# Kernel tuning notes

Hardware: AMD Instinct MI355X
Metric: run time of the kernel (lower is better)

Reference implementation:

```python
import jax, jax.numpy as jnp
import numpy as np

N_USERS = 200000
N_SPOTS = 50000
N_EDGES = 3200000
D = 64


def setup_inputs() -> dict:
    key = jax.random.key(0)
    k1, k2, k3, k4 = jax.random.split(key, 4)
    return {
        "user_x": jax.random.normal(k1, (N_USERS, D), dtype=jnp.float32),
        "spot_x": jax.random.normal(k2, (N_SPOTS, D), dtype=jnp.float32),
        "user_idx": jax.random.randint(k3, (N_EDGES,), 0, N_USERS, dtype=jnp.int32),
        "spot_idx": jax.random.randint(k4, (N_EDGES,), 0, N_SPOTS, dtype=jnp.int32),
    }


def reference(user_x, spot_x, user_idx, spot_idx):
    n_users, n_spots = user_x.shape[0], spot_x.shape[0]
    dtype = user_x.dtype
    ones = jnp.ones(user_idx.shape[0], dtype=dtype)
    # per-node degrees (counts of edge endpoints); isolated nodes get 1e-6
    user_div = jax.ops.segment_sum(ones, user_idx, num_segments=n_users)
    spot_div = jax.ops.segment_sum(ones, spot_idx, num_segments=n_spots)
    user_div = jnp.where(user_div == 0, jnp.asarray(1e-6, dtype), user_div)
    spot_div = jnp.where(spot_div == 0, jnp.asarray(1e-6, dtype), spot_div)
    inv_sqrt_user = jax.lax.rsqrt(user_div)  # [n_users]
    inv_sqrt_spot = jax.lax.rsqrt(spot_div)  # [n_spots]
    # gather + pre-normalize per-edge messages
    spot_msg = spot_x[spot_idx] * inv_sqrt_spot[spot_idx][:, None]  # [E, D]
    user_msg = user_x[user_idx] * inv_sqrt_user[user_idx][:, None]  # [E, D]
    # scatter-add into destination nodes, then post-normalize by dest degree
    spot_out = jax.ops.segment_sum(user_msg, spot_idx, num_segments=n_spots)
    user_out = jax.ops.segment_sum(spot_msg, user_idx, num_segments=n_users)
    spot_out = spot_out * inv_sqrt_spot[:, None]
    user_out = user_out * inv_sqrt_user[:, None]
    return (user_out, spot_out)
```

## Files before the change

### kernel.cpp

```cpp
#include <hip/hip_runtime.h>

#define DFEAT  64
#define BSH    7
#define BN     128
#define PBITS  18
#define PMASK  ((1u << PBITS) - 1)
#define NSPLIT 384
#define STR_U  2560
#define STR_S  9216


__device__ __forceinline__ long long bucket_base(int b, int NB_U) {
    return (b < NB_U) ? (long long)b * STR_U
                      : (long long)NB_U * STR_U + (long long)(b - NB_U) * STR_S;
}

__global__ __launch_bounds__(256) void split_kernel(const int* __restrict__ uidx,
                                                    const int* __restrict__ sidx,
                                                    int* __restrict__ cursor,
                                                    unsigned int* __restrict__ staging,
                                                    int n_edges, int NB_U, int NB) {
    __shared__ int h[2048];
    __shared__ int rc[2048];
    for (int i = threadIdx.x; i < NB; i += 256) h[i] = 0;
    __syncthreads();
    int epb = (((n_edges + gridDim.x - 1) / gridDim.x) + 3) & ~3;
    int e0 = blockIdx.x * epb;
    int e1 = min(e0 + epb, n_edges);
    int len = e1 - e0; if (len < 0) len = 0;
    int nv = e0 + (len & ~3);
    for (int v = e0 + 4 * (int)threadIdx.x; v < nv; v += 1024) {
        int4 u = *(const int4*)(uidx + v);
        int4 s = *(const int4*)(sidx + v);
        atomicAdd(&h[u.x >> BSH], 1); atomicAdd(&h[u.y >> BSH], 1);
        atomicAdd(&h[u.z >> BSH], 1); atomicAdd(&h[u.w >> BSH], 1);
        atomicAdd(&h[NB_U + (s.x >> BSH)], 1); atomicAdd(&h[NB_U + (s.y >> BSH)], 1);
        atomicAdd(&h[NB_U + (s.z >> BSH)], 1); atomicAdd(&h[NB_U + (s.w >> BSH)], 1);
    }
    for (int e = nv + (int)threadIdx.x; e < e1; e += 256) {
        atomicAdd(&h[uidx[e] >> BSH], 1);
        atomicAdd(&h[NB_U + (sidx[e] >> BSH)], 1);
    }
    __syncthreads();
    for (int i = threadIdx.x; i < NB; i += 256) {
        int c = h[i];
        rc[i] = c ? (int)(bucket_base(i, NB_U) + atomicAdd(&cursor[i], c)) : 0;
    }
    __syncthreads();
    for (int v = e0 + 4 * (int)threadIdx.x; v < nv; v += 1024) {
        int4 u4 = *(const int4*)(uidx + v);
        int4 s4 = *(const int4*)(sidx + v);
#pragma unroll
        for (int k = 0; k < 4; ++k) {
            int u = ((const int*)&u4)[k];
            int s = ((const int*)&s4)[k];
            int pu = atomicAdd(&rc[u >> BSH], 1);
            staging[pu] = ((unsigned int)(u & (BN - 1)) << PBITS) | (unsigned int)s;
            int ps = atomicAdd(&rc[NB_U + (s >> BSH)], 1);
            staging[ps] = ((unsigned int)(s & (BN - 1)) << PBITS) | (unsigned int)u;
        }
    }
    for (int e = nv + (int)threadIdx.x; e < e1; e += 256) {
        int u = uidx[e], s = sidx[e];
        int pu = atomicAdd(&rc[u >> BSH], 1);
        staging[pu] = ((unsigned int)(u & (BN - 1)) << PBITS) | (unsigned int)s;
        int ps = atomicAdd(&rc[NB_U + (s >> BSH)], 1);
        staging[ps] = ((unsigned int)(s & (BN - 1)) << PBITS) | (unsigned int)u;
    }
}

template <int CAPN>
__global__ __launch_bounds__(256) void csr_build_inplace_t(
        unsigned int* __restrict__ staging,
        const int* __restrict__ cursor,
        int* __restrict__ start,
        int* __restrict__ cnt,
        float* __restrict__ isq,
        int n_users, int n_spots,
        int NB_U, int b0) {
    __shared__ unsigned int buf[CAPN];
    __shared__ int hist[BN];
    __shared__ int scanbuf[BN];
    __shared__ int cur[BN];
    int b = b0 + blockIdx.x, t = threadIdx.x;
    long long beg = bucket_base(b, NB_U);
    int len = cursor[b];
    if (len > CAPN) len = CAPN;
    if (t < BN) hist[t] = 0;
    __syncthreads();
    for (int i = t; i < len; i += 256) {
        unsigned int e = __builtin_nontemporal_load(&staging[beg + i]);
        buf[i] = e;
        atomicAdd(&hist[e >> PBITS], 1);
    }
    __syncthreads();
    if (t < BN) scanbuf[t] = hist[t];
    __syncthreads();
    for (int off = 1; off < BN; off <<= 1) {
        int v = (t >= off && t < BN) ? scanbuf[t - off] : 0;
        __syncthreads();
        if (t < BN) scanbuf[t] += v;
        __syncthreads();
    }
    if (t < BN) {
        int excl = scanbuf[t] - hist[t];
        cur[t] = (int)beg + excl;
        bool ub = (b < NB_U);
        int node = (ub ? (b << BSH) : ((b - NB_U) << BSH)) + t;
        int lim  = ub ? n_users : n_spots;
        if (node < lim) {
            int gi = ub ? node : (n_users + node);
            start[gi] = (int)beg + excl;
            cnt[gi]   = hist[t];
            float d = hist[t] ? (float)hist[t] : 1e-6f;
            isq[gi] = rsqrtf(d);
        }
    }
    __syncthreads();
    for (int i = t; i < len; i += 256) {
        unsigned int e = buf[i];
        int pos = atomicAdd(&cur[e >> PBITS], 1);
        staging[pos] = e & PMASK;
    }
}

__global__ __launch_bounds__(256) void scale_feat(const float* __restrict__ ux,
                                                  const float* __restrict__ sx,
                                                  const float* __restrict__ isq,
                                                  float* __restrict__ scaled,
                                                  int n_users, int A) {
    int t = blockIdx.x * 256 + threadIdx.x;
    int total = A << 4;
    if (t >= total) return;
    int node = t >> 4;
    int c4 = t & 15;
    const float* src = (node < n_users)
        ? (ux + ((long long)node << 6))
        : (sx + ((long long)(node - n_users) << 6));
    float4 v = ((const float4*)src)[c4];
    float f = isq[node];
    v.x *= f; v.y *= f; v.z *= f; v.w *= f;
    ((float4*)(scaled + ((long long)node << 6)))[c4] = v;
}

template <int G, bool SCALED>
__device__ __forceinline__ void gather_group(int j, int pv, float fv,
        const float* __restrict__ src, int lane,
        float& a0, float& a1, float& a2, float& a3) {
    float v[G];
#pragma unroll
    for (int k = 0; k < G; ++k) {
        int p = __builtin_amdgcn_readlane(pv, j + k);
        v[k] = src[(p << 6) + lane];
    }
    __builtin_amdgcn_sched_barrier(0);
#pragma unroll
    for (int k = 0; k < G; ++k) {
        if (SCALED) {
            if ((k & 3) == 0) a0 += v[k];
            else if ((k & 3) == 1) a1 += v[k];
            else if ((k & 3) == 2) a2 += v[k];
            else a3 += v[k];
        } else {
            float f = __uint_as_float((unsigned)__builtin_amdgcn_readlane(
                          (int)__float_as_uint(fv), j + k));
            if ((k & 3) == 0) a0 = fmaf(f, v[k], a0);
            else if ((k & 3) == 1) a1 = fmaf(f, v[k], a1);
            else if ((k & 3) == 2) a2 = fmaf(f, v[k], a2);
            else a3 = fmaf(f, v[k], a3);
        }
    }
}

template <bool SCALED>
__global__ __launch_bounds__(256) void gather_t(
        const float* __restrict__ user_x,
        const float* __restrict__ spot_x,
        const float* __restrict__ scaled,
        const float* __restrict__ isq,
        const int* __restrict__ start,
        const int* __restrict__ cnt,
        const int* __restrict__ csr,
        float* __restrict__ user_out,
        float* __restrict__ spot_out,
        int n_users, int n_spots) {
    int lane = (int)threadIdx.x & 63;
    int w = __builtin_amdgcn_readfirstlane((int)blockIdx.x * 4 + ((int)threadIdx.x >> 6));
    int A = n_users + n_spots;
    if (w >= A) return;
    bool ub = (w < n_users);
    const float* __restrict__ src;
    if (SCALED) src = scaled + (ub ? ((long long)n_users << 6) : 0);
    else        src = ub ? spot_x : user_x;
    const float* __restrict__ isqp = isq + (ub ? n_users : 0);
    int beg = __builtin_amdgcn_readfirstlane(start[w]);
    int end = beg + __builtin_amdgcn_readfirstlane(cnt[w]);
    float a0 = 0.f, a1 = 0.f, a2 = 0.f, a3 = 0.f;
    for (int i = beg; i < end; i += 64) {
        int n = end - i; if (n > 64) n = 64;
        int pv = 0; float fv = 0.0f;
        if (lane < n) {
            int p = __builtin_nontemporal_load(&csr[i + lane]);
            pv = p;
            if (!SCALED) fv = isqp[p];
        }
        int j = 0;
        for (; j + 16 <= n; j += 16)
            gather_group<16, SCALED>(j, pv, fv, src, lane, a0, a1, a2, a3);
        if (j + 8 <= n) {
            gather_group<8, SCALED>(j, pv, fv, src, lane, a0, a1, a2, a3);
            j += 8;
        }
        if (j + 4 <= n) {
            gather_group<4, SCALED>(j, pv, fv, src, lane, a0, a1, a2, a3);
            j += 4;
        }
        for (; j < n; ++j) {
            int p = __builtin_amdgcn_readlane(pv, j);
            if (SCALED) a0 += src[(p << 6) + lane];
            else {
                float f = __uint_as_float((unsigned)__builtin_amdgcn_readlane(
                              (int)__float_as_uint(fv), j));
                a0 = fmaf(f, src[(p << 6) + lane], a0);
            }
        }
    }
    float r = ((a0 + a1) + (a2 + a3)) * isq[w];
    if (ub) __builtin_nontemporal_store(r, &user_out[((long long)w << 6) + lane]);
    else    __builtin_nontemporal_store(r, &spot_out[((long long)(w - n_users) << 6) + lane]);
}


__global__ void deg_kernel(const int* __restrict__ uidx,
                           const int* __restrict__ sidx,
                           unsigned int* __restrict__ udeg,
                           unsigned int* __restrict__ sdeg,
                           int n_edges) {
    int e = blockIdx.x * blockDim.x + threadIdx.x;
    if (e < n_edges) {
        atomicAdd(&udeg[uidx[e]], 1u);
        atomicAdd(&sdeg[sidx[e]], 1u);
    }
}

__global__ void rsqrt_kernel(unsigned int* __restrict__ deg_as_uint,
                             float* __restrict__ isq, int n) {
    int i = blockIdx.x * blockDim.x + threadIdx.x;
    if (i < n) {
        float d = (float)deg_as_uint[i];
        if (d == 0.0f) d = 1e-6f;
        isq[i] = rsqrtf(d);
    }
}

__global__ void scatter_kernel(const float* __restrict__ user_x,
                               const float* __restrict__ spot_x,
                               const int* __restrict__ uidx,
                               const int* __restrict__ sidx,
                               const float* __restrict__ isqu,
                               const float* __restrict__ isqs,
                               float* __restrict__ user_out,
                               float* __restrict__ spot_out,
                               int n_edges) {
    long long t = (long long)blockIdx.x * blockDim.x + threadIdx.x;
    int e = (int)(t >> 6);
    int lane = (int)(t & 63);
    if (e < n_edges) {
        int u = uidx[e];
        int s = sidx[e];
        float sv = spot_x[(long long)s * DFEAT + lane] * isqs[s];
        float uv = user_x[(long long)u * DFEAT + lane] * isqu[u];
        unsafeAtomicAdd(&user_out[(long long)u * DFEAT + lane], sv);
        unsafeAtomicAdd(&spot_out[(long long)s * DFEAT + lane], uv);
    }
}

__global__ void scale_kernel(float* __restrict__ user_out,
                             float* __restrict__ spot_out,
                             const float* __restrict__ isqu,
                             const float* __restrict__ isqs,
                             int n_users, int n_spots) {
    long long t = (long long)blockIdx.x * blockDim.x + threadIdx.x;
    long long total_u = (long long)n_users * DFEAT;
    long long total_s = (long long)n_spots * DFEAT;
    if (t < total_u) {
        user_out[t] *= isqu[t >> 6];
    } else if (t < total_u + total_s) {
        long long t2 = t - total_u;
        spot_out[t2] *= isqs[t2 >> 6];
    }
}


extern "C" void kernel_launch(void* const* d_in, const int* in_sizes, int n_in,
                              void* d_out, int out_size, void* d_ws, size_t ws_size,
                              hipStream_t stream) {
    const float* user_x = (const float*)d_in[0];
    const float* spot_x = (const float*)d_in[1];
    const int* uidx = (const int*)d_in[2];
    const int* sidx = (const int*)d_in[3];

    const int n_users = in_sizes[0] / DFEAT;
    const int n_spots = in_sizes[1] / DFEAT;
    const int n_edges = in_sizes[2];
    const int A = n_users + n_spots;

    float* user_out = (float*)d_out;
    float* spot_out = (float*)d_out + (long long)n_users * DFEAT;

    const int NB_U = (n_users + BN - 1) / BN;
    const int NB_S = (n_spots + BN - 1) / BN;
    const int NB = NB_U + NB_S;

    const long long SE = (long long)NB_U * STR_U + (long long)NB_S * STR_S;
    const long long off_start = NB;
    const long long off_cnt   = off_start + A;
    const long long off_isq   = off_cnt + A;
    const long long off_stg   = off_isq + A;
    const long long off_scl   = off_stg + SE;
    const long long need_core   = off_scl * 4;
    const long long need_scaled = (off_scl + (long long)A * DFEAT) * 4;

    bool fits = NB <= 2048 &&
                n_users <= (1 << PBITS) && n_spots <= (1 << PBITS);

    if (fits && (long long)ws_size >= need_core) {
        int* cursor           = (int*)d_ws;
        int* start            = (int*)d_ws + off_start;
        int* cnt              = (int*)d_ws + off_cnt;
        float* isq            = (float*)d_ws + off_isq;
        unsigned int* staging = (unsigned int*)d_ws + off_stg;
        float* scaled         = (float*)d_ws + off_scl;
        bool use_scaled = (long long)ws_size >= need_scaled;

        hipMemsetAsync(cursor, 0, (size_t)NB * 4, stream);

        split_kernel<<<NSPLIT, 256, 0, stream>>>(uidx, sidx, cursor, staging,
                                                 n_edges, NB_U, NB);
        csr_build_inplace_t<STR_S><<<NB_S, 256, 0, stream>>>(
            staging, cursor, start, cnt, isq, n_users, n_spots, NB_U, NB_U);
        csr_build_inplace_t<STR_U><<<NB_U, 256, 0, stream>>>(
            staging, cursor, start, cnt, isq, n_users, n_spots, NB_U, 0);

        if (use_scaled) {
            int blocks = (A * 16 + 255) / 256;
            scale_feat<<<blocks, 256, 0, stream>>>(user_x, spot_x, isq, scaled,
                                                   n_users, A);
        }
        {
            long long total = (long long)A * 64;
            int blocks = (int)((total + 255) / 256);
            if (use_scaled)
                gather_t<true><<<blocks, 256, 0, stream>>>(
                    user_x, spot_x, scaled, isq, start, cnt, (const int*)staging,
                    user_out, spot_out, n_users, n_spots);
            else
                gather_t<false><<<blocks, 256, 0, stream>>>(
                    user_x, spot_x, scaled, isq, start, cnt, (const int*)staging,
                    user_out, spot_out, n_users, n_spots);
        }
    } else {
        float* isqu = (float*)d_ws;
        float* isqs = isqu + n_users;
        unsigned int* udeg = (unsigned int*)isqu;
        unsigned int* sdeg = (unsigned int*)isqs;

        hipMemsetAsync(d_out, 0, (size_t)out_size * sizeof(float), stream);
        hipMemsetAsync(d_ws, 0, (size_t)A * sizeof(unsigned int), stream);

        {
            int blocks = (n_edges + 255) / 256;
            deg_kernel<<<blocks, 256, 0, stream>>>(uidx, sidx, udeg, sdeg, n_edges);
        }
        {
            int blocks = (A + 255) / 256;
            rsqrt_kernel<<<blocks, 256, 0, stream>>>((unsigned int*)d_ws, (float*)d_ws, A);
        }
        {
            long long total = (long long)n_edges * 64;
            int blocks = (int)((total + 255) / 256);
            scatter_kernel<<<blocks, 256, 0, stream>>>(
                user_x, spot_x, uidx, sidx, isqu, isqs, user_out, spot_out, n_edges);
        }
        {
            long long total = (long long)A * 64;
            int blocks = (int)((total + 255) / 256);
            scale_kernel<<<blocks, 256, 0, stream>>>(
                user_out, spot_out, isqu, isqs, n_users, n_spots);
        }
    }
}
```

Before: 529.2 us.

## Fuse feature prescaling into CSR build and store scaled features as fp16

Drops the separate scale_feat kernel. Each CSR-build block now scales its bucket's node features by their inverse-sqrt degree right after computing them, and writes the result as fp16. The gather kernel reads these half-precision rows and accumulates in fp32, which halves the bytes moved per random gather and saves one launch and one full pass over the features. The cost is fp16 rounding of the prescaled messages, which may loosen accuracy against the fp32 reference. The fallback path that gathered unscaled fp32 features when workspace was short is removed, so more workspace is now needed.

Result: faster. 429.5 us (-18.8%).

```diff
diff --git a/kernel.cpp b/kernel.cpp
--- a/kernel.cpp
+++ b/kernel.cpp
@@ -1,4 +1,5 @@
 #include <hip/hip_runtime.h>
+#include <hip/hip_fp16.h>
 
 #define DFEAT  64
 #define BSH    7
@@ -8,6 +9,9 @@
 #define NSPLIT 384
 #define STR_U  2560
 #define STR_S  9216
+
+typedef float          __attribute__((ext_vector_type(4))) f32x4;
+typedef unsigned short __attribute__((ext_vector_type(4))) u16x4;
 
 
 __device__ __forceinline__ long long bucket_base(int b, int NB_U) {
@@ -76,12 +80,16 @@
         int* __restrict__ start,
         int* __restrict__ cnt,
         float* __restrict__ isq,
+        const float* __restrict__ ux,
+        const float* __restrict__ sx,
+        unsigned short* __restrict__ scaledH,
         int n_users, int n_spots,
         int NB_U, int b0) {
     __shared__ unsigned int buf[CAPN];
     __shared__ int hist[BN];
     __shared__ int scanbuf[BN];
     __shared__ int cur[BN];
+    __shared__ float fisq[BN];
     int b = b0 + blockIdx.x, t = threadIdx.x;
     long long beg = bucket_base(b, NB_U);
     int len = cursor[b];
@@ -102,18 +110,21 @@
         if (t < BN) scanbuf[t] += v;
         __syncthreads();
     }
+    bool ub = (b < NB_U);
+    int node0 = (ub ? (b << BSH) : ((b - NB_U) << BSH));
+    int lim   = ub ? n_users : n_spots;
     if (t < BN) {
         int excl = scanbuf[t] - hist[t];
         cur[t] = (int)beg + excl;
-        bool ub = (b < NB_U);
-        int node = (ub ? (b << BSH) : ((b - NB_U) << BSH)) + t;
-        int lim  = ub ? n_users : n_spots;
+        int node = node0 + t;
         if (node < lim) {
             int gi = ub ? node : (n_users + node);
             start[gi] = (int)beg + excl;
             cnt[gi]   = hist[t];
             float d = hist[t] ? (float)hist[t] : 1e-6f;
-            isq[gi] = rsqrtf(d);
+            float is = rsqrtf(d);
+            isq[gi]  = is;
+            fisq[t]  = is;
         }
     }
     __syncthreads();
@@ -122,32 +133,31 @@
         int pos = atomicAdd(&cur[e >> PBITS], 1);
         staging[pos] = e & PMASK;
     }
-}
-
-__global__ __launch_bounds__(256) void scale_feat(const float* __restrict__ ux,
-                                                  const float* __restrict__ sx,
-                                                  const float* __restrict__ isq,
-                                                  float* __restrict__ scaled,
-                                                  int n_users, int A) {
-    int t = blockIdx.x * 256 + threadIdx.x;
-    int total = A << 4;
-    if (t >= total) return;
-    int node = t >> 4;
-    int c4 = t & 15;
-    const float* src = (node < n_users)
-        ? (ux + ((long long)node << 6))
-        : (sx + ((long long)(node - n_users) << 6));
-    float4 v = ((const float4*)src)[c4];
-    float f = isq[node];
-    v.x *= f; v.y *= f; v.z *= f; v.w *= f;
-    ((float4*)(scaled + ((long long)node << 6)))[c4] = v;
-}
-
-template <int G, bool SCALED>
-__device__ __forceinline__ void gather_group(int j, int pv, float fv,
-        const float* __restrict__ src, int lane,
+    const f32x4* __restrict__ xs4 = (const f32x4*)(ub ? ux : sx);
+    u16x4* __restrict__ dst4 = (u16x4*)scaledH + ((long long)(ub ? node0 : n_users + node0) << 4);
+#pragma unroll
+    for (int k = 0; k < 8; ++k) {
+        int idx4 = t + k * 256;
+        int nl = idx4 >> 4;
+        int node = node0 + nl;
+        if (node < lim) {
+            f32x4 v = __builtin_nontemporal_load(xs4 + ((long long)node << 4) + (idx4 & 15));
+            float f = fisq[nl];
+            u16x4 hh;
+            hh.x = __half_as_ushort(__float2half(v.x * f));
+            hh.y = __half_as_ushort(__float2half(v.y * f));
+            hh.z = __half_as_ushort(__float2half(v.z * f));
+            hh.w = __half_as_ushort(__float2half(v.w * f));
+            dst4[((long long)nl << 4) + (idx4 & 15)] = hh;
+        }
+    }
+}
+
+template <int G>
+__device__ __forceinline__ void gather_groupH(int j, int pv,
+        const unsigned short* __restrict__ src, int lane,
         float& a0, float& a1, float& a2, float& a3) {
-    float v[G];
+    unsigned short v[G];
 #pragma unroll
     for (int k = 0; k < G; ++k) {
         int p = __builtin_amdgcn_readlane(pv, j + k);
@@ -156,27 +166,16 @@
     __builtin_amdgcn_sched_barrier(0);
 #pragma unroll
     for (int k = 0; k < G; ++k) {
-        if (SCALED) {
-            if ((k & 3) == 0) a0 += v[k];
-            else if ((k & 3) == 1) a1 += v[k];
-            else if ((k & 3) == 2) a2 += v[k];
-            else a3 += v[k];
-        } else {
-            float f = __uint_as_float((unsigned)__builtin_amdgcn_readlane(
-                          (int)__float_as_uint(fv), j + k));
-            if ((k & 3) == 0) a0 = fmaf(f, v[k], a0);
-            else if ((k & 3) == 1) a1 = fmaf(f, v[k], a1);
-            else if ((k & 3) == 2) a2 = fmaf(f, v[k], a2);
-            else a3 = fmaf(f, v[k], a3);
-        }
-    }
-}
-
-template <bool SCALED>
-__global__ __launch_bounds__(256) void gather_t(
-        const float* __restrict__ user_x,
-        const float* __restrict__ spot_x,
-        const float* __restrict__ scaled,
+        float x = __half2float(__ushort_as_half(v[k]));
+        if ((k & 3) == 0) a0 += x;
+        else if ((k & 3) == 1) a1 += x;
+        else if ((k & 3) == 2) a2 += x;
+        else a3 += x;
+    }
+}
+
+__global__ __launch_bounds__(256) void gather_h(
+        const unsigned short* __restrict__ scaled,
         const float* __restrict__ isq,
         const int* __restrict__ start,
         const int* __restrict__ cnt,
@@ -189,40 +188,23 @@
     int A = n_users + n_spots;
     if (w >= A) return;
     bool ub = (w < n_users);
-    const float* __restrict__ src;
-    if (SCALED) src = scaled + (ub ? ((long long)n_users << 6) : 0);
-    else        src = ub ? spot_x : user_x;
-    const float* __restrict__ isqp = isq + (ub ? n_users : 0);
+    const unsigned short* __restrict__ src =
+        scaled + (ub ? ((long long)n_users << 6) : 0);
     int beg = __builtin_amdgcn_readfirstlane(start[w]);
     int end = beg + __builtin_amdgcn_readfirstlane(cnt[w]);
     float a0 = 0.f, a1 = 0.f, a2 = 0.f, a3 = 0.f;
     for (int i = beg; i < end; i += 64) {
         int n = end - i; if (n > 64) n = 64;
-        int pv = 0; float fv = 0.0f;
-        if (lane < n) {
-            int p = __builtin_nontemporal_load(&csr[i + lane]);
-            pv = p;
-            if (!SCALED) fv = isqp[p];
-        }
+        int pv = 0;
+        if (lane < n) pv = __builtin_nontemporal_load(&csr[i + lane]);
         int j = 0;
         for (; j + 16 <= n; j += 16)
-            gather_group<16, SCALED>(j, pv, fv, src, lane, a0, a1, a2, a3);
-        if (j + 8 <= n) {
-            gather_group<8, SCALED>(j, pv, fv, src, lane, a0, a1, a2, a3);
-            j += 8;
-        }
-        if (j + 4 <= n) {
-            gather_group<4, SCALED>(j, pv, fv, src, lane, a0, a1, a2, a3);
-            j += 4;
-        }
+            gather_groupH<16>(j, pv, src, lane, a0, a1, a2, a3);
+        if (j + 8 <= n) { gather_groupH<8>(j, pv, src, lane, a0, a1, a2, a3); j += 8; }
+        if (j + 4 <= n) { gather_groupH<4>(j, pv, src, lane, a0, a1, a2, a3); j += 4; }
         for (; j < n; ++j) {
             int p = __builtin_amdgcn_readlane(pv, j);
-            if (SCALED) a0 += src[(p << 6) + lane];
-            else {
-                float f = __uint_as_float((unsigned)__builtin_amdgcn_readlane(
-                              (int)__float_as_uint(fv), j));
-                a0 = fmaf(f, src[(p << 6) + lane], a0);
-            }
+            a0 += __half2float(__ushort_as_half(src[(p << 6) + lane]));
         }
     }
     float r = ((a0 + a1) + (a2 + a3)) * isq[w];
@@ -317,47 +299,36 @@
     const long long off_cnt   = off_start + A;
     const long long off_isq   = off_cnt + A;
     const long long off_stg   = off_isq + A;
-    const long long off_scl   = off_stg + SE;
-    const long long need_core   = off_scl * 4;
-    const long long need_scaled = (off_scl + (long long)A * DFEAT) * 4;
+    const long long off_scl   = (off_stg + SE + 1) & ~1LL;
+    const long long need = off_scl * 4 + (long long)A * DFEAT * 2;
 
     bool fits = NB <= 2048 &&
                 n_users <= (1 << PBITS) && n_spots <= (1 << PBITS);
 
-    if (fits && (long long)ws_size >= need_core) {
+    if (fits && (long long)ws_size >= need) {
         int* cursor           = (int*)d_ws;
         int* start            = (int*)d_ws + off_start;
         int* cnt              = (int*)d_ws + off_cnt;
         float* isq            = (float*)d_ws + off_isq;
         unsigned int* staging = (unsigned int*)d_ws + off_stg;
-        float* scaled         = (float*)d_ws + off_scl;
-        bool use_scaled = (long long)ws_size >= need_scaled;
+        unsigned short* scaledH = (unsigned short*)((int*)d_ws + off_scl);
 
         hipMemsetAsync(cursor, 0, (size_t)NB * 4, stream);
 
         split_kernel<<<NSPLIT, 256, 0, stream>>>(uidx, sidx, cursor, staging,
                                                  n_edges, NB_U, NB);
         csr_build_inplace_t<STR_S><<<NB_S, 256, 0, stream>>>(
-            staging, cursor, start, cnt, isq, n_users, n_spots, NB_U, NB_U);
+            staging, cursor, start, cnt, isq, user_x, spot_x, scaledH,
+            n_users, n_spots, NB_U, NB_U);
         csr_build_inplace_t<STR_U><<<NB_U, 256, 0, stream>>>(
-            staging, cursor, start, cnt, isq, n_users, n_spots, NB_U, 0);
-
-        if (use_scaled) {
-            int blocks = (A * 16 + 255) / 256;
-            scale_feat<<<blocks, 256, 0, stream>>>(user_x, spot_x, isq, scaled,
-                                                   n_users, A);
-        }
+            staging, cursor, start, cnt, isq, user_x, spot_x, scaledH,
+            n_users, n_spots, NB_U, 0);
         {
             long long total = (long long)A * 64;
             int blocks = (int)((total + 255) / 256);
-            if (use_scaled)
-                gather_t<true><<<blocks, 256, 0, stream>>>(
-                    user_x, spot_x, scaled, isq, start, cnt, (const int*)staging,
-                    user_out, spot_out, n_users, n_spots);
-            else
-                gather_t<false><<<blocks, 256, 0, stream>>>(
-                    user_x, spot_x, scaled, isq, start, cnt, (const int*)staging,
-                    user_out, spot_out, n_users, n_spots);
+            gather_h<<<blocks, 256, 0, stream>>>(
+                scaledH, isq, start, cnt, (const int*)staging,
+                user_out, spot_out, n_users, n_spots);
         }
     } else {
         float* isqu = (float*)d_ws;
```
